# Kernel tuning notes

Hardware: AMD Instinct MI355X
Metric: run time of the kernel (lower is better)

Reference implementation:

```python
import jax, jax.numpy as jnp
import numpy as np

N_SRC = 20000
N_TGT = 20000
N_EDGE = 320000
D = 128            # in_dim == hid_dim
EDGE_IN = 2 * D + 1  # src feat + tgt feat + radial
COORD_MAX = 10.0


def _mlp2(x, w1, b1, w2, b2):
    # Linear -> SiLU -> Linear -> SiLU (edge MLP)
    h = jax.nn.silu(x @ w1 + b1)
    return jax.nn.silu(h @ w2 + b2)


def setup_inputs() -> dict:
    key = jax.random.key(0)
    ks = jax.random.split(key, 32)
    s = 0.05
    inp = {
        "src_node_feat": jax.random.normal(ks[0], (N_SRC, D), jnp.float32),
        "tgt_node_feat": jax.random.normal(ks[1], (N_TGT, D), jnp.float32),
        "src_node_coord": jax.random.normal(ks[2], (N_SRC, 3), jnp.float32),
        "tgt_node_coord": jax.random.normal(ks[3], (N_TGT, 3), jnp.float32),
        "edge_src": jax.random.randint(ks[4], (N_EDGE,), 0, N_SRC, jnp.int32),
        "edge_tgt": jax.random.randint(ks[5], (N_EDGE,), 0, N_TGT, jnp.int32),
        # edge MLP s2t
        "w1_s2t": jax.random.normal(ks[6], (EDGE_IN, D), jnp.float32) * s,
        "b1_s2t": jnp.zeros((D,), jnp.float32),
        "w2_s2t": jax.random.normal(ks[7], (D, D), jnp.float32) * s,
        "b2_s2t": jnp.zeros((D,), jnp.float32),
        # edge MLP t2s
        "w1_t2s": jax.random.normal(ks[8], (EDGE_IN, D), jnp.float32) * s,
        "b1_t2s": jnp.zeros((D,), jnp.float32),
        "w2_t2s": jax.random.normal(ks[9], (D, D), jnp.float32) * s,
        "b2_t2s": jnp.zeros((D,), jnp.float32),
        # gate MLPs (Linear(D,1) + Sigmoid)
        "wg_s2t": jax.random.normal(ks[10], (D, 1), jnp.float32) * s,
        "bg_s2t": jnp.zeros((1,), jnp.float32),
        "wg_t2s": jax.random.normal(ks[11], (D, 1), jnp.float32) * s,
        "bg_t2s": jnp.zeros((1,), jnp.float32),
        # coord MLP: Linear(D,D) + SiLU + Linear(D,1, bias=False, xavier gain 1e-3)
        "wc1": jax.random.normal(ks[12], (D, D), jnp.float32) * s,
        "bc1": jnp.zeros((D,), jnp.float32),
        "wc2": jax.random.normal(ks[13], (D, 1), jnp.float32) * 0.001,
        # node MLP tgt: Linear(2D,D) + SiLU + Linear(D,D)
        "wn1_t": jax.random.normal(ks[14], (2 * D, D), jnp.float32) * s,
        "bn1_t": jnp.zeros((D,), jnp.float32),
        "wn2_t": jax.random.normal(ks[15], (D, D), jnp.float32) * s,
        "bn2_t": jnp.zeros((D,), jnp.float32),
        # node MLP src
        "wn1_s": jax.random.normal(ks[16], (2 * D, D), jnp.float32) * s,
        "bn1_s": jnp.zeros((D,), jnp.float32),
        "wn2_s": jax.random.normal(ks[17], (D, D), jnp.float32) * s,
        "bn2_s": jnp.zeros((D,), jnp.float32),
    }
    return inp


def reference(src_node_feat, tgt_node_feat, src_node_coord, tgt_node_coord,
              edge_src, edge_tgt,
              w1_s2t, b1_s2t, w2_s2t, b2_s2t,
              w1_t2s, b1_t2s, w2_t2s, b2_t2s,
              wg_s2t, bg_s2t, wg_t2s, bg_t2s,
              wc1, bc1, wc2,
              wn1_t, bn1_t, wn2_t, bn2_t,
              wn1_s, bn1_s, wn2_s, bn2_s):
    # ---- coord2radial ----
    coord_diff = tgt_node_coord[edge_tgt] - src_node_coord[edge_src]  # [E,3]
    radial = jnp.sum(coord_diff ** 2, axis=1, keepdims=True)          # [E,1]

    # ---- edge function (gather + concat + two edge MLPs + gates) ----
    edge_in = jnp.concatenate(
        [src_node_feat[edge_src], tgt_node_feat[edge_tgt], radial], axis=1)  # [E, 257]
    e_s2t = _mlp2(edge_in, w1_s2t, b1_s2t, w2_s2t, b2_s2t)  # [E,D]
    e_t2s = _mlp2(edge_in, w1_t2s, b1_t2s, w2_t2s, b2_t2s)  # [E,D]
    e_s2t = e_s2t * jax.nn.sigmoid(e_s2t @ wg_s2t + bg_s2t)
    e_t2s = e_t2s * jax.nn.sigmoid(e_t2s @ wg_t2s + bg_t2s)

    # ---- coord update (coords_agg='mean', output_coord=True) ----
    coord_w = jax.nn.silu(e_s2t @ wc1 + bc1) @ wc2          # [E,1]
    weighted_trans = coord_diff * coord_w                   # [E,3]
    trans_sum = jax.ops.segment_sum(weighted_trans, edge_tgt, num_segments=N_TGT)
    cnt = jax.ops.segment_sum(jnp.ones((weighted_trans.shape[0],), jnp.float32),
                              edge_tgt, num_segments=N_TGT)
    agg_trans = trans_sum / jnp.maximum(cnt, 1.0)[:, None]
    tgt_coord_out = tgt_node_coord + jnp.clip(agg_trans, -COORD_MAX, COORD_MAX)

    # ---- node function (scatter-add aggregation + node MLPs + residual) ----
    agg_s2t = jax.ops.segment_sum(e_s2t, edge_tgt, num_segments=N_TGT)  # [Nt,D]
    agg_t2s = jax.ops.segment_sum(e_t2s, edge_src, num_segments=N_SRC)  # [Ns,D]
    tgt_in = jnp.concatenate([tgt_node_feat, agg_s2t], axis=1)  # [Nt,2D]
    src_in = jnp.concatenate([src_node_feat, agg_t2s], axis=1)  # [Ns,2D]
    tgt_out = jax.nn.silu(tgt_in @ wn1_t + bn1_t) @ wn2_t + bn2_t
    src_out = jax.nn.silu(src_in @ wn1_s + bn1_s) @ wn2_s + bn2_s
    tgt_out = tgt_node_feat + tgt_out  # residual (dims match)
    src_out = src_node_feat + src_out

    return src_out, tgt_out, src_node_coord, tgt_coord_out
```

## Files before the change

### kernel.cpp

```cpp
#include <hip/hip_runtime.h>

#define NN 20000
#define NEDGE 320000
#define COORD_MAX 10.0f

#define LDH 136
#define TILE_N 64
#define LDN  264

typedef __attribute__((ext_vector_type(4))) float f32x4;
typedef __attribute__((ext_vector_type(8))) short short8;
typedef __attribute__((ext_vector_type(8))) __bf16 bf16x8;

static __device__ __forceinline__ f32x4 mfma16(short8 a, short8 b, f32x4 c) {
  return __builtin_amdgcn_mfma_f32_16x16x32_bf16(
      __builtin_bit_cast(bf16x8, a), __builtin_bit_cast(bf16x8, b), c, 0, 0, 0);
}
static __device__ __forceinline__ unsigned short f2bf(float f) {
  unsigned u = __builtin_bit_cast(unsigned, f);
  u += 0x7FFFu + ((u >> 16) & 1u);
  return (unsigned short)(u >> 16);
}
static __device__ __forceinline__ float bf2f(unsigned short u) {
  unsigned x = ((unsigned)u) << 16;
  return __builtin_bit_cast(float, x);
}
static __device__ __forceinline__ unsigned cvtpk(float lo, float hi) {
  unsigned r;
  asm("v_cvt_pk_bf16_f32 %0, %1, %2" : "=v"(r) : "v"(lo), "v"(hi));
  return r;
}
static __device__ __forceinline__ float sigm(float x) {
  return __builtin_amdgcn_rcpf(1.f + __expf(-x));
}
static __device__ __forceinline__ float silu_(float x) { return x * sigm(x); }

struct PackJobs {
  const float* w[11];
  unsigned short* o[11];
  int kreal[11];
  int nk[11];
};

__global__ void egnn_pack_all(PackJobs J) {
  const int job = blockIdx.y;
  const int nk = J.nk[job];
  const int idx = blockIdx.x * 256 + threadIdx.x;
  if (idx >= nk * 512) return;
  const float* w = J.w[job];
  const int kreal = J.kreal[job];
  const int lane = idx & 63;
  const int ct = (idx >> 6) & 7;
  const int kstep = idx >> 9;
  const int col = ct * 16 + (lane & 15);
  const int k0 = kstep * 32 + (lane >> 4) * 8;
  union { short8 s; unsigned short u[8]; } t;
#pragma unroll
  for (int j = 0; j < 8; ++j) {
    int k = k0 + j;
    t.u[j] = (k < kreal) ? f2bf(w[(size_t)k * 128 + col]) : (unsigned short)0;
  }
  reinterpret_cast<short8*>(J.o[job])[idx] = t.s;
}

struct PreJobs {
  const float* x[4];
  const unsigned short* w[4];
  unsigned short* o[4];
};

__global__ __launch_bounds__(256, 2) void egnn_pre(PreJobs J, int N) {
  __shared__ __align__(16) unsigned short sX[64 * LDH];
  const int job = blockIdx.y;
  const float* X = J.x[job];
  const unsigned short* W = J.w[job];
  unsigned short* O = J.o[job];
  const int n0 = blockIdx.x * 64;
  const int tid = threadIdx.x;

  for (int s = tid; s < 64 * 32; s += 256) {
    const int row = s >> 5;
    const int c4 = (s & 31) * 4;
    const int node = n0 + row;
    float4 v = {0.f, 0.f, 0.f, 0.f};
    if (node < N) v = reinterpret_cast<const float4*>(X + (size_t)node * 128)[s & 31];
    *reinterpret_cast<uint2*>(&sX[row * LDH + c4]) =
        uint2{cvtpk(v.x, v.y), cvtpk(v.z, v.w)};
  }
  __syncthreads();

  const int lane = tid & 63, wid = tid >> 6;
  const int r16 = lane & 15, g4 = lane >> 4;
  const int rowBase = wid * 16;

  f32x4 acc[8];
#pragma unroll
  for (int ct = 0; ct < 8; ++ct) acc[ct] = f32x4{0.f, 0.f, 0.f, 0.f};
#pragma unroll
  for (int ks = 0; ks < 4; ++ks) {
    const short8 a = *reinterpret_cast<const short8*>(
        &sX[(rowBase + r16) * LDH + ks * 32 + g4 * 8]);
#pragma unroll
    for (int ct = 0; ct < 8; ++ct) {
      const short8 b = *reinterpret_cast<const short8*>(
          W + ((size_t)(ks * 8 + ct) * 64 + lane) * 8);
      acc[ct] = mfma16(a, b, acc[ct]);
    }
  }
#pragma unroll
  for (int ct = 0; ct < 8; ++ct) {
    const int col = ct * 16 + r16;
#pragma unroll
    for (int r = 0; r < 4; ++r) {
      const int node = n0 + rowBase + g4 * 4 + r;
      if (node < N) O[(size_t)node * 128 + col] = f2bf(acc[ct][r]);
    }
  }
}

__global__ void egnn_hist(const int* __restrict__ eTgt, const int* __restrict__ eSrc,
                          int* __restrict__ cntT, int* __restrict__ cntS) {
  const int e = blockIdx.x * 256 + threadIdx.x;
  if (e < NEDGE) {
    atomicAdd(&cntT[eTgt[e]], 1);
    atomicAdd(&cntS[eSrc[e]], 1);
  }
}

__global__ __launch_bounds__(1024) void egnn_scan(
    const int* __restrict__ c0, int* __restrict__ r0, int* __restrict__ o0,
    const int* __restrict__ c1, int* __restrict__ r1, int* __restrict__ o1, int n) {
  const int* cnt = blockIdx.x ? c1 : c0;
  int* rp = blockIdx.x ? r1 : r0;
  int* oc = blockIdx.x ? o1 : o0;
  __shared__ int sums[1024];
  const int tid = threadIdx.x;
  const int chunk = (n + 1023) / 1024;
  const int i0 = tid * chunk;
  int local = 0;
  for (int k = 0; k < chunk; ++k) {
    const int i = i0 + k;
    if (i < n) local += cnt[i];
  }
  sums[tid] = local;
  __syncthreads();
  for (int s = 1; s < 1024; s <<= 1) {
    int v = (tid >= s) ? sums[tid - s] : 0;
    __syncthreads();
    sums[tid] += v;
    __syncthreads();
  }
  int run = (tid == 0) ? 0 : sums[tid - 1];
  for (int k = 0; k < chunk; ++k) {
    const int i = i0 + k;
    if (i < n) { rp[i] = run; oc[i] = run; run += cnt[i]; }
  }
  if (tid == 1023) rp[n] = sums[1023];
}

__global__ void egnn_scatter(const int* __restrict__ eTgt, const int* __restrict__ eSrc,
                             int* __restrict__ offT, int* __restrict__ offS,
                             int* __restrict__ permT, int* __restrict__ permS) {
  const int e = blockIdx.x * 256 + threadIdx.x;
  if (e < NEDGE) {
    permT[atomicAdd(&offT[eTgt[e]], 1)] = e;
    permS[atomicAdd(&offS[eSrc[e]], 1)] = e;
  }
}

__global__ __launch_bounds__(256, 4) void egnn_edge(
    const unsigned short* __restrict__ S1A, const unsigned short* __restrict__ T1A,
    const unsigned short* __restrict__ S1B, const unsigned short* __restrict__ T1B,
    const float* __restrict__ srcC, const float* __restrict__ tgtC,
    const int* __restrict__ eSrc, const int* __restrict__ eTgt,
    const float* __restrict__ w1A, const float* __restrict__ b1A,
    const float* __restrict__ w1B, const float* __restrict__ b1B,
    const unsigned short* __restrict__ w2pA, const float* __restrict__ b2A,
    const float* __restrict__ wgA, const float* __restrict__ bgA,
    const unsigned short* __restrict__ w2pB, const float* __restrict__ b2B,
    const float* __restrict__ wgB, const float* __restrict__ bgB,
    const unsigned short* __restrict__ wc1p, const float* __restrict__ bc1,
    const float* __restrict__ wc2,
    const int* __restrict__ permT, const int* __restrict__ permS,
    float* __restrict__ aggA, float* __restrict__ aggB,
    float* __restrict__ wtBuf)
{
  __shared__ __align__(16) unsigned short sH[4][32 * LDH];
  __shared__ float sCD[128 * 3];
  __shared__ float sRad[128];
  __shared__ int sS[128];
  __shared__ int sT[128];

  const int dir = blockIdx.y;
  const int tid = threadIdx.x;
  const int j0 = blockIdx.x * 128;
  const int* __restrict__ perm = dir ? permS : permT;

  if (tid < 128) {
    const int e = perm[j0 + tid];
    const int s = eSrc[e], t = eTgt[e];
    sS[tid] = s; sT[tid] = t;
    const float dx = tgtC[t * 3 + 0] - srcC[s * 3 + 0];
    const float dy = tgtC[t * 3 + 1] - srcC[s * 3 + 1];
    const float dz = tgtC[t * 3 + 2] - srcC[s * 3 + 2];
    sCD[tid * 3 + 0] = dx; sCD[tid * 3 + 1] = dy; sCD[tid * 3 + 2] = dz;
    sRad[tid] = dx * dx + dy * dy + dz * dz;
  }
  __syncthreads();

  const int lane = tid & 63, wid = tid >> 6;
  const int r16 = lane & 15, g4 = lane >> 4;
  const int we = wid * 32;
  const int h32 = lane >> 5;
  const int c4 = (lane & 31) * 4;

  const unsigned short* S1 = dir ? S1B : S1A;
  const unsigned short* T1 = dir ? T1B : T1A;
  const float* w1 = dir ? w1B : w1A;
  const float* b1 = dir ? b1B : b1A;
  const float4 wr = *reinterpret_cast<const float4*>(w1 + 256 * 128 + c4);
  const float4 bb = *reinterpret_cast<const float4*>(b1 + c4);

  unsigned short* hT = sH[wid];

#pragma unroll 8
  for (int i = 0; i < 16; ++i) {
    const int row = 2 * i + h32;
    const int e = we + row;
    const int s = sS[e], t = sT[e];
    const float rad = sRad[e];
    const ushort4 a = *reinterpret_cast<const ushort4*>(S1 + (size_t)s * 128 + c4);
    const ushort4 b = *reinterpret_cast<const ushort4*>(T1 + (size_t)t * 128 + c4);
    const float f0 = silu_(bf2f(a.x) + bf2f(b.x) + rad * wr.x + bb.x);
    const float f1 = silu_(bf2f(a.y) + bf2f(b.y) + rad * wr.y + bb.y);
    const float f2 = silu_(bf2f(a.z) + bf2f(b.z) + rad * wr.z + bb.z);
    const float f3 = silu_(bf2f(a.w) + bf2f(b.w) + rad * wr.w + bb.w);
    *reinterpret_cast<uint2*>(&hT[row * LDH + c4]) =
        uint2{cvtpk(f0, f1), cvtpk(f2, f3)};
  }

  const unsigned short* w2p = dir ? w2pB : w2pA;
  f32x4 acc[2][8];
#pragma unroll
  for (int rt = 0; rt < 2; ++rt)
#pragma unroll
    for (int ct = 0; ct < 8; ++ct) acc[rt][ct] = f32x4{0.f, 0.f, 0.f, 0.f};
#pragma unroll
  for (int ks = 0; ks < 4; ++ks) {
    short8 a[2];
#pragma unroll
    for (int rt = 0; rt < 2; ++rt)
      a[rt] = *reinterpret_cast<const short8*>(
          &hT[(rt * 16 + r16) * LDH + ks * 32 + g4 * 8]);
#pragma unroll
    for (int ct = 0; ct < 8; ++ct) {
      const short8 b = *reinterpret_cast<const short8*>(
          w2p + ((size_t)(ks * 8 + ct) * 64 + lane) * 8);
#pragma unroll
      for (int rt = 0; rt < 2; ++rt) acc[rt][ct] = mfma16(a[rt], b, acc[rt][ct]);
    }
  }

  const float* b2 = dir ? b2B : b2A;
  const float* wg = dir ? wgB : wgA;
  const float bg = dir ? bgB[0] : bgA[0];
  float part[2][4];
#pragma unroll
  for (int rt = 0; rt < 2; ++rt)
#pragma unroll
    for (int r = 0; r < 4; ++r) part[rt][r] = 0.f;
#pragma unroll
  for (int ct = 0; ct < 8; ++ct) {
    const float b2v = b2[ct * 16 + r16];
    const float wgv = wg[ct * 16 + r16];
#pragma unroll
    for (int rt = 0; rt < 2; ++rt)
#pragma unroll
      for (int r = 0; r < 4; ++r) {
        const float e = silu_(acc[rt][ct][r] + b2v);
        acc[rt][ct][r] = e;
        part[rt][r] += e * wgv;
      }
  }
#pragma unroll
  for (int m = 1; m < 16; m <<= 1)
#pragma unroll
    for (int rt = 0; rt < 2; ++rt)
#pragma unroll
      for (int r = 0; r < 4; ++r) part[rt][r] += __shfl_xor(part[rt][r], m, 64);
#pragma unroll
  for (int rt = 0; rt < 2; ++rt)
#pragma unroll
    for (int r = 0; r < 4; ++r) {
      const float gate = sigm(part[rt][r] + bg);
#pragma unroll
      for (int ct = 0; ct < 8; ++ct) acc[rt][ct][r] *= gate;
    }

#pragma unroll
  for (int rt = 0; rt < 2; ++rt)
#pragma unroll
    for (int ct = 0; ct < 8; ++ct)
#pragma unroll
      for (int r = 0; r < 4; ++r)
        hT[(rt * 16 + g4 * 4 + r) * LDH + ct * 16 + r16] = f2bf(acc[rt][ct][r]);

  if (dir == 0) {
    f32x4 ac[2][8];
#pragma unroll
    for (int rt = 0; rt < 2; ++rt)
#pragma unroll
      for (int ct = 0; ct < 8; ++ct) ac[rt][ct] = f32x4{0.f, 0.f, 0.f, 0.f};
#pragma unroll
    for (int ks = 0; ks < 4; ++ks) {
      short8 a[2];
#pragma unroll
      for (int rt = 0; rt < 2; ++rt)
        a[rt] = *reinterpret_cast<const short8*>(
            &hT[(rt * 16 + r16) * LDH + ks * 32 + g4 * 8]);
#pragma unroll
      for (int ct = 0; ct < 8; ++ct) {
        const short8 b = *reinterpret_cast<const short8*>(
            wc1p + ((size_t)(ks * 8 + ct) * 64 + lane) * 8);
#pragma unroll
        for (int rt = 0; rt < 2; ++rt) ac[rt][ct] = mfma16(a[rt], b, ac[rt][ct]);
      }
    }
    float pc[2][4];
#pragma unroll
    for (int rt = 0; rt < 2; ++rt)
#pragma unroll
      for (int r = 0; r < 4; ++r) pc[rt][r] = 0.f;
#pragma unroll
    for (int ct = 0; ct < 8; ++ct) {
      const float bcv = bc1[ct * 16 + r16];
      const float w2v = wc2[ct * 16 + r16];
#pragma unroll
      for (int rt = 0; rt < 2; ++rt)
#pragma unroll
        for (int r = 0; r < 4; ++r)
          pc[rt][r] += silu_(ac[rt][ct][r] + bcv) * w2v;
    }
#pragma unroll
    for (int m = 1; m < 16; m <<= 1)
#pragma unroll
      for (int rt = 0; rt < 2; ++rt)
#pragma unroll
        for (int r = 0; r < 4; ++r) pc[rt][r] += __shfl_xor(pc[rt][r], m, 64);

#pragma unroll
    for (int rt = 0; rt < 2; ++rt)
#pragma unroll
      for (int r = 0; r < 4; ++r) {
        if (r16 == 0) {
          const int el = we + rt * 16 + g4 * 4 + r;
          const float p = pc[rt][r];
          const float4 w = {sCD[el * 3 + 0] * p, sCD[el * 3 + 1] * p,
                            sCD[el * 3 + 2] * p, 0.f};
          *reinterpret_cast<float4*>(wtBuf + (size_t)(j0 + el) * 4) = w;
        }
      }
  }

  {
    const int* __restrict__ nids = dir ? sS : sT;
    float* __restrict__ agg = dir ? aggB : aggA;
    const int c2 = lane * 2;
    float s0 = 0.f, s1 = 0.f;
    int curNode = nids[we];
    int segStart = 0;
#pragma unroll 4
    for (int row = 0; row < 32; ++row) {
      const ushort2 v = *reinterpret_cast<const ushort2*>(&hT[row * LDH + c2]);
      s0 += bf2f(v.x); s1 += bf2f(v.y);
      const int nxt = (row < 31) ? nids[we + row + 1] : -1;
      if (nxt != curNode) {
        float* dst = agg + (size_t)curNode * 128 + c2;
        if (segStart > 0 && row < 31) {
          dst[0] = s0; dst[1] = s1;
        } else {
          atomicAdd(dst, s0);
          atomicAdd(dst + 1, s1);
        }
        s0 = 0.f; s1 = 0.f;
        curNode = nxt; segStart = row + 1;
      }
    }
  }
}

__global__ void egnn_coord(const float* __restrict__ srcC, const float* __restrict__ tgtC,
                           const float* __restrict__ wt, const int* __restrict__ rp,
                           float* __restrict__ outSC, float* __restrict__ outTC) {
  const int n = blockIdx.x * 256 + threadIdx.x;
  if (n >= NN) return;
  outSC[n * 3 + 0] = srcC[n * 3 + 0];
  outSC[n * 3 + 1] = srcC[n * 3 + 1];
  outSC[n * 3 + 2] = srcC[n * 3 + 2];
  const int j0 = rp[n], j1 = rp[n + 1];
  float ax = 0.f, ay = 0.f, az = 0.f;
  for (int j = j0; j < j1; ++j) {
    const float4 v = *reinterpret_cast<const float4*>(wt + (size_t)j * 4);
    ax += v.x; ay += v.y; az += v.z;
  }
  const float c = fmaxf((float)(j1 - j0), 1.f);
  ax = fminf(fmaxf(ax / c, -COORD_MAX), COORD_MAX);
  ay = fminf(fmaxf(ay / c, -COORD_MAX), COORD_MAX);
  az = fminf(fmaxf(az / c, -COORD_MAX), COORD_MAX);
  outTC[n * 3 + 0] = tgtC[n * 3 + 0] + ax;
  outTC[n * 3 + 1] = tgtC[n * 3 + 1] + ay;
  outTC[n * 3 + 2] = tgtC[n * 3 + 2] + az;
}

struct NodeJobs {
  const float* feat[2];
  const float* agg[2];
  const unsigned short* w1p[2];
  const float* b1[2];
  const unsigned short* w2p[2];
  const float* b2[2];
  float* outp[2];
};

__global__ __launch_bounds__(256, 2) void egnn_node(NodeJobs J, int N) {
  __shared__ __align__(16) unsigned short sIn[TILE_N * LDN];
  __shared__ __align__(16) unsigned short sH2[TILE_N * LDH];
  const int job = blockIdx.y;
  const float* __restrict__ feat = J.feat[job];
  const float* __restrict__ agg = J.agg[job];
  const unsigned short* __restrict__ w1p = J.w1p[job];
  const float* __restrict__ b1 = J.b1[job];
  const unsigned short* __restrict__ w2p = J.w2p[job];
  const float* __restrict__ b2 = J.b2[job];
  float* __restrict__ outp = J.outp[job];

  const int tid = threadIdx.x;
  const int n0 = blockIdx.x * TILE_N;

  for (int s = tid; s < 64 * 64; s += 256) {
    const int row = s >> 6;
    const int half = (s >> 5) & 1;
    const int c4 = (s & 31) * 4;
    const int node = n0 + row;
    float4 v = {0.f, 0.f, 0.f, 0.f};
    if (node < N)
      v = reinterpret_cast<const float4*>((half ? agg : feat) + (size_t)node * 128)[s & 31];
    *reinterpret_cast<uint2*>(&sIn[row * LDN + half * 128 + c4]) =
        uint2{cvtpk(v.x, v.y), cvtpk(v.z, v.w)};
  }
  __syncthreads();

  const int lane = tid & 63;
  const int wid = tid >> 6;
  const int rowBase = wid * 16;
  const int r16 = lane & 15;
  const int g4 = lane >> 4;

  f32x4 acc[8];
#pragma unroll
  for (int ct = 0; ct < 8; ++ct) acc[ct] = f32x4{0.f, 0.f, 0.f, 0.f};
#pragma unroll
  for (int ks = 0; ks < 8; ++ks) {
    const short8 a = *reinterpret_cast<const short8*>(
        &sIn[(rowBase + r16) * LDN + ks * 32 + g4 * 8]);
#pragma unroll
    for (int ct = 0; ct < 8; ++ct) {
      const short8 b = *reinterpret_cast<const short8*>(
          w1p + ((size_t)(ks * 8 + ct) * 64 + lane) * 8);
      acc[ct] = mfma16(a, b, acc[ct]);
    }
  }
#pragma unroll
  for (int ct = 0; ct < 8; ++ct) {
    const int col = ct * 16 + r16;
    const float bias = b1[col];
#pragma unroll
    for (int r = 0; r < 4; ++r) {
      const float h = silu_(acc[ct][r] + bias);
      sH2[(rowBase + g4 * 4 + r) * LDH + col] = f2bf(h);
    }
  }

  f32x4 acc2[8];
#pragma unroll
  for (int ct = 0; ct < 8; ++ct) acc2[ct] = f32x4{0.f, 0.f, 0.f, 0.f};
#pragma unroll
  for (int ks = 0; ks < 4; ++ks) {
    const short8 a = *reinterpret_cast<const short8*>(
        &sH2[(rowBase + r16) * LDH + ks * 32 + g4 * 8]);
#pragma unroll
    for (int ct = 0; ct < 8; ++ct) {
      const short8 b = *reinterpret_cast<const short8*>(
          w2p + ((size_t)(ks * 8 + ct) * 64 + lane) * 8);
      acc2[ct] = mfma16(a, b, acc2[ct]);
    }
  }

#pragma unroll
  for (int ct = 0; ct < 8; ++ct) {
    const int col = ct * 16 + r16;
    const float bias = b2[col];
#pragma unroll
    for (int r = 0; r < 4; ++r) {
      const int node = n0 + rowBase + g4 * 4 + r;
      if (node < N)
        outp[(size_t)node * 128 + col] = feat[(size_t)node * 128 + col] + acc2[ct][r] + bias;
    }
  }
}

extern "C" void kernel_launch(void* const* d_in, const int* in_sizes, int n_in,
                              void* d_out, int out_size, void* d_ws, size_t ws_size,
                              hipStream_t stream) {
  const float* srcF = (const float*)d_in[0];
  const float* tgtF = (const float*)d_in[1];
  const float* srcC = (const float*)d_in[2];
  const float* tgtC = (const float*)d_in[3];
  const int* eSrc = (const int*)d_in[4];
  const int* eTgt = (const int*)d_in[5];
  const float* w1_s2t = (const float*)d_in[6];
  const float* b1_s2t = (const float*)d_in[7];
  const float* w2_s2t = (const float*)d_in[8];
  const float* b2_s2t = (const float*)d_in[9];
  const float* w1_t2s = (const float*)d_in[10];
  const float* b1_t2s = (const float*)d_in[11];
  const float* w2_t2s = (const float*)d_in[12];
  const float* b2_t2s = (const float*)d_in[13];
  const float* wg_s2t = (const float*)d_in[14];
  const float* bg_s2t = (const float*)d_in[15];
  const float* wg_t2s = (const float*)d_in[16];
  const float* bg_t2s = (const float*)d_in[17];
  const float* wc1 = (const float*)d_in[18];
  const float* bc1 = (const float*)d_in[19];
  const float* wc2 = (const float*)d_in[20];
  const float* wn1_t = (const float*)d_in[21];
  const float* bn1_t = (const float*)d_in[22];
  const float* wn2_t = (const float*)d_in[23];
  const float* bn2_t = (const float*)d_in[24];
  const float* wn1_s = (const float*)d_in[25];
  const float* bn1_s = (const float*)d_in[26];
  const float* wn2_s = (const float*)d_in[27];
  const float* bn2_s = (const float*)d_in[28];

  char* ws = (char*)d_ws;
  size_t off = 0;
  auto take = [&](size_t bytes) -> char* {
    char* p = ws + off;
    off = (off + bytes + 255) & ~(size_t)255;
    return p;
  };
  float* aggA = (float*)take((size_t)NN * 128 * 4);
  float* aggB = (float*)take((size_t)NN * 128 * 4);
  float* wtBuf = (float*)take((size_t)NEDGE * 4 * 4);
  unsigned short* S1A = (unsigned short*)take((size_t)NN * 128 * 2);
  unsigned short* T1A = (unsigned short*)take((size_t)NN * 128 * 2);
  unsigned short* S1B = (unsigned short*)take((size_t)NN * 128 * 2);
  unsigned short* T1B = (unsigned short*)take((size_t)NN * 128 * 2);
  unsigned short* w1tA = (unsigned short*)take(4 * 4096 * 2);
  unsigned short* w1mA = (unsigned short*)take(4 * 4096 * 2);
  unsigned short* w1tB = (unsigned short*)take(4 * 4096 * 2);
  unsigned short* w1mB = (unsigned short*)take(4 * 4096 * 2);
  unsigned short* w2pA = (unsigned short*)take(4 * 4096 * 2);
  unsigned short* w2pB = (unsigned short*)take(4 * 4096 * 2);
  unsigned short* wc1p = (unsigned short*)take(4 * 4096 * 2);
  unsigned short* wn1pt = (unsigned short*)take(8 * 4096 * 2);
  unsigned short* wn2pt = (unsigned short*)take(4 * 4096 * 2);
  unsigned short* wn1ps = (unsigned short*)take(8 * 4096 * 2);
  unsigned short* wn2ps = (unsigned short*)take(4 * 4096 * 2);
  int* cntT = (int*)take((size_t)NN * 4);
  int* cntS = (int*)take((size_t)NN * 4);
  const char* cntZeroStart = (const char*)cntT;
  const size_t cntZeroBytes = (size_t)((char*)cntS + NN * 4 - (char*)cntT);
  int* rowptrT = (int*)take((size_t)(NN + 1) * 4);
  int* rowptrS = (int*)take((size_t)(NN + 1) * 4);
  int* offT = (int*)take((size_t)NN * 4);
  int* offS = (int*)take((size_t)NN * 4);
  int* permT = (int*)take((size_t)NEDGE * 4);
  int* permS = (int*)take((size_t)NEDGE * 4);

  hipMemsetAsync(aggA, 0, (size_t)NN * 128 * 4 * 2, stream);
  hipMemsetAsync((void*)cntZeroStart, 0, cntZeroBytes, stream);

  PackJobs PJ;
  PJ.w[0] = w1_s2t;             PJ.o[0] = w1tA;  PJ.kreal[0] = 128; PJ.nk[0] = 4;
  PJ.w[1] = w1_s2t + 128 * 128; PJ.o[1] = w1mA;  PJ.kreal[1] = 128; PJ.nk[1] = 4;
  PJ.w[2] = w1_t2s;             PJ.o[2] = w1tB;  PJ.kreal[2] = 128; PJ.nk[2] = 4;
  PJ.w[3] = w1_t2s + 128 * 128; PJ.o[3] = w1mB;  PJ.kreal[3] = 128; PJ.nk[3] = 4;
  PJ.w[4] = w2_s2t;             PJ.o[4] = w2pA;  PJ.kreal[4] = 128; PJ.nk[4] = 4;
  PJ.w[5] = w2_t2s;             PJ.o[5] = w2pB;  PJ.kreal[5] = 128; PJ.nk[5] = 4;
  PJ.w[6] = wc1;                PJ.o[6] = wc1p;  PJ.kreal[6] = 128; PJ.nk[6] = 4;
  PJ.w[7] = wn1_t;              PJ.o[7] = wn1pt; PJ.kreal[7] = 256; PJ.nk[7] = 8;
  PJ.w[8] = wn2_t;              PJ.o[8] = wn2pt; PJ.kreal[8] = 128; PJ.nk[8] = 4;
  PJ.w[9] = wn1_s;              PJ.o[9] = wn1ps; PJ.kreal[9] = 256; PJ.nk[9] = 8;
  PJ.w[10] = wn2_s;             PJ.o[10] = wn2ps; PJ.kreal[10] = 128; PJ.nk[10] = 4;
  egnn_pack_all<<<dim3(16, 11), 256, 0, stream>>>(PJ);

  PreJobs PR;
  PR.x[0] = srcF; PR.w[0] = w1tA; PR.o[0] = S1A;
  PR.x[1] = tgtF; PR.w[1] = w1mA; PR.o[1] = T1A;
  PR.x[2] = srcF; PR.w[2] = w1tB; PR.o[2] = S1B;
  PR.x[3] = tgtF; PR.w[3] = w1mB; PR.o[3] = T1B;
  egnn_pre<<<dim3(313, 4), 256, 0, stream>>>(PR, NN);

  egnn_hist<<<NEDGE / 256, 256, 0, stream>>>(eTgt, eSrc, cntT, cntS);
  egnn_scan<<<2, 1024, 0, stream>>>(cntT, rowptrT, offT, cntS, rowptrS, offS, NN);
  egnn_scatter<<<NEDGE / 256, 256, 0, stream>>>(eTgt, eSrc, offT, offS, permT, permS);

  float* outSrc = (float*)d_out;
  float* outTgt = outSrc + (size_t)NN * 128;
  float* outSC  = outTgt + (size_t)NN * 128;
  float* outTC  = outSC + (size_t)NN * 3;

  egnn_edge<<<dim3(NEDGE / 128, 2), 256, 0, stream>>>(
      S1A, T1A, S1B, T1B, srcC, tgtC, eSrc, eTgt,
      w1_s2t, b1_s2t, w1_t2s, b1_t2s,
      w2pA, b2_s2t, wg_s2t, bg_s2t,
      w2pB, b2_t2s, wg_t2s, bg_t2s,
      wc1p, bc1, wc2, permT, permS, aggA, aggB, wtBuf);

  egnn_coord<<<(NN + 255) / 256, 256, 0, stream>>>(
      srcC, tgtC, wtBuf, rowptrT, outSC, outTC);

  NodeJobs NJ;
  NJ.feat[0] = tgtF; NJ.agg[0] = aggA;
  NJ.w1p[0] = wn1pt; NJ.b1[0] = bn1_t; NJ.w2p[0] = wn2pt; NJ.b2[0] = bn2_t;
  NJ.outp[0] = outTgt;
  NJ.feat[1] = srcF; NJ.agg[1] = aggB;
  NJ.w1p[1] = wn1ps; NJ.b1[1] = bn1_s; NJ.w2p[1] = wn2ps; NJ.b2[1] = bn2_s;
  NJ.outp[1] = outSrc;

  const int nodeBlocks = (NN + TILE_N - 1) / TILE_N;
  egnn_node<<<dim3(nodeBlocks, 2), 256, 0, stream>>>(NJ, NN);
}
```

Measured before the change: 320.9 us.

## Merge small kernels, fold first-layer bias into precompute, widen edge gather loads

Histogram, weight packing and aggregation zeroing now run in one prep launch. The coordinate reduction moves into the node kernel as a third grid row, which removes launches and the separate memset. The pre-projection now processes both directions per block, reusing the staged input tile, and adds the first-layer bias into the target projection so the edge kernel no longer adds it. The edge gather uses 16-byte loads of 8 bf16 values per lane instead of 8-byte loads. The prep grid is much larger, and most blocks in the pack rows exit immediately, which adds some idle work.

```diff
diff --git a/kernel.cpp b/kernel.cpp
--- a/kernel.cpp
+++ b/kernel.cpp
@@ -42,39 +42,56 @@
   int nk[11];
 };
 
-__global__ void egnn_pack_all(PackJobs J) {
+__global__ void egnn_prep(PackJobs J,
+                          const int* __restrict__ eTgt, const int* __restrict__ eSrc,
+                          int* __restrict__ cntT, int* __restrict__ cntS,
+                          float* __restrict__ aggZero ) {
   const int job = blockIdx.y;
-  const int nk = J.nk[job];
   const int idx = blockIdx.x * 256 + threadIdx.x;
-  if (idx >= nk * 512) return;
-  const float* w = J.w[job];
-  const int kreal = J.kreal[job];
-  const int lane = idx & 63;
-  const int ct = (idx >> 6) & 7;
-  const int kstep = idx >> 9;
-  const int col = ct * 16 + (lane & 15);
-  const int k0 = kstep * 32 + (lane >> 4) * 8;
-  union { short8 s; unsigned short u[8]; } t;
-#pragma unroll
-  for (int j = 0; j < 8; ++j) {
-    int k = k0 + j;
-    t.u[j] = (k < kreal) ? f2bf(w[(size_t)k * 128 + col]) : (unsigned short)0;
-  }
-  reinterpret_cast<short8*>(J.o[job])[idx] = t.s;
+  if (job < 11) {
+    const int nk = J.nk[job];
+    if (idx >= nk * 512) return;
+    const float* w = J.w[job];
+    const int kreal = J.kreal[job];
+    const int lane = idx & 63;
+    const int ct = (idx >> 6) & 7;
+    const int kstep = idx >> 9;
+    const int col = ct * 16 + (lane & 15);
+    const int k0 = kstep * 32 + (lane >> 4) * 8;
+    union { short8 s; unsigned short u[8]; } t;
+#pragma unroll
+    for (int j = 0; j < 8; ++j) {
+      int k = k0 + j;
+      t.u[j] = (k < kreal) ? f2bf(w[(size_t)k * 128 + col]) : (unsigned short)0;
+    }
+    reinterpret_cast<short8*>(J.o[job])[idx] = t.s;
+  } else if (job == 11) {
+    if (idx < NEDGE) {
+      atomicAdd(&cntT[eTgt[idx]], 1);
+      atomicAdd(&cntS[eSrc[idx]], 1);
+    }
+  } else {
+    float4* p = reinterpret_cast<float4*>(aggZero);
+    const int total = 2 * NN * 128 / 4;
+    for (int k = idx; k < total; k += 1250 * 256)
+      p[k] = float4{0.f, 0.f, 0.f, 0.f};
+  }
 }
 
 struct PreJobs {
-  const float* x[4];
-  const unsigned short* w[4];
-  unsigned short* o[4];
+  const float* x[2];
+  const unsigned short* wA[2];
+  const unsigned short* wB[2];
+  const float* biasA[2];
+  const float* biasB[2];
+  unsigned short* oA[2];
+  unsigned short* oB[2];
 };
 
 __global__ __launch_bounds__(256, 2) void egnn_pre(PreJobs J, int N) {
   __shared__ __align__(16) unsigned short sX[64 * LDH];
   const int job = blockIdx.y;
-  const float* X = J.x[job];
-  const unsigned short* W = J.w[job];
-  unsigned short* O = J.o[job];
+  const float* __restrict__ X = J.x[job];
   const int n0 = blockIdx.x * 64;
   const int tid = threadIdx.x;
 
@@ -93,37 +110,35 @@
   const int r16 = lane & 15, g4 = lane >> 4;
   const int rowBase = wid * 16;
 
-  f32x4 acc[8];
-#pragma unroll
-  for (int ct = 0; ct < 8; ++ct) acc[ct] = f32x4{0.f, 0.f, 0.f, 0.f};
-#pragma unroll
-  for (int ks = 0; ks < 4; ++ks) {
-    const short8 a = *reinterpret_cast<const short8*>(
-        &sX[(rowBase + r16) * LDH + ks * 32 + g4 * 8]);
+#pragma unroll 1
+  for (int half = 0; half < 2; ++half) {
+    const unsigned short* __restrict__ W = half ? J.wB[job] : J.wA[job];
+    const float* __restrict__ bias = half ? J.biasB[job] : J.biasA[job];
+    unsigned short* __restrict__ O = half ? J.oB[job] : J.oA[job];
+    f32x4 acc[8];
+#pragma unroll
+    for (int ct = 0; ct < 8; ++ct) acc[ct] = f32x4{0.f, 0.f, 0.f, 0.f};
+#pragma unroll
+    for (int ks = 0; ks < 4; ++ks) {
+      const short8 a = *reinterpret_cast<const short8*>(
+          &sX[(rowBase + r16) * LDH + ks * 32 + g4 * 8]);
+#pragma unroll
+      for (int ct = 0; ct < 8; ++ct) {
+        const short8 b = *reinterpret_cast<const short8*>(
+            W + ((size_t)(ks * 8 + ct) * 64 + lane) * 8);
+        acc[ct] = mfma16(a, b, acc[ct]);
+      }
+    }
 #pragma unroll
     for (int ct = 0; ct < 8; ++ct) {
-      const short8 b = *reinterpret_cast<const short8*>(
-          W + ((size_t)(ks * 8 + ct) * 64 + lane) * 8);
-      acc[ct] = mfma16(a, b, acc[ct]);
-    }
-  }
-#pragma unroll
-  for (int ct = 0; ct < 8; ++ct) {
-    const int col = ct * 16 + r16;
-#pragma unroll
-    for (int r = 0; r < 4; ++r) {
-      const int node = n0 + rowBase + g4 * 4 + r;
-      if (node < N) O[(size_t)node * 128 + col] = f2bf(acc[ct][r]);
-    }
-  }
-}
-
-__global__ void egnn_hist(const int* __restrict__ eTgt, const int* __restrict__ eSrc,
-                          int* __restrict__ cntT, int* __restrict__ cntS) {
-  const int e = blockIdx.x * 256 + threadIdx.x;
-  if (e < NEDGE) {
-    atomicAdd(&cntT[eTgt[e]], 1);
-    atomicAdd(&cntS[eSrc[e]], 1);
+      const int col = ct * 16 + r16;
+      const float bv = bias ? bias[col] : 0.f;
+#pragma unroll
+      for (int r = 0; r < 4; ++r) {
+        const int node = n0 + rowBase + g4 * 4 + r;
+        if (node < N) O[(size_t)node * 128 + col] = f2bf(acc[ct][r] + bv);
+      }
+    }
   }
 }
 
@@ -173,8 +188,7 @@
     const unsigned short* __restrict__ S1B, const unsigned short* __restrict__ T1B,
     const float* __restrict__ srcC, const float* __restrict__ tgtC,
     const int* __restrict__ eSrc, const int* __restrict__ eTgt,
-    const float* __restrict__ w1A, const float* __restrict__ b1A,
-    const float* __restrict__ w1B, const float* __restrict__ b1B,
+    const float* __restrict__ w1A, const float* __restrict__ w1B,
     const unsigned short* __restrict__ w2pA, const float* __restrict__ b2A,
     const float* __restrict__ wgA, const float* __restrict__ bgA,
     const unsigned short* __restrict__ w2pB, const float* __restrict__ b2B,
@@ -213,30 +227,42 @@
   const int we = wid * 32;
   const int h32 = lane >> 5;
   const int c4 = (lane & 31) * 4;
-
-  const unsigned short* S1 = dir ? S1B : S1A;
-  const unsigned short* T1 = dir ? T1B : T1A;
+  const int c8 = (lane & 15) * 8;
+  const int r4 = lane >> 4;
+  const int c2 = lane * 2;
+
+  const unsigned short* __restrict__ S1 = dir ? S1B : S1A;
+  const unsigned short* __restrict__ T1 = dir ? T1B : T1A;
   const float* w1 = dir ? w1B : w1A;
-  const float* b1 = dir ? b1B : b1A;
-  const float4 wr = *reinterpret_cast<const float4*>(w1 + 256 * 128 + c4);
-  const float4 bb = *reinterpret_cast<const float4*>(b1 + c4);
+  const float4 wr0 = *reinterpret_cast<const float4*>(w1 + 256 * 128 + c8);
+  const float4 wr1 = *reinterpret_cast<const float4*>(w1 + 256 * 128 + c8 + 4);
+  const float* b2 = dir ? b2B : b2A;
+  const float* wg = dir ? wgB : wgA;
+  const float bg = dir ? bgB[0] : bgA[0];
+  const int* __restrict__ nids = dir ? sS : sT;
+  float* __restrict__ agg = dir ? aggB : aggA;
 
   unsigned short* hT = sH[wid];
 
-#pragma unroll 8
-  for (int i = 0; i < 16; ++i) {
-    const int row = 2 * i + h32;
+#pragma unroll
+  for (int i = 0; i < 8; ++i) {
+    const int row = 4 * i + r4;
     const int e = we + row;
     const int s = sS[e], t = sT[e];
     const float rad = sRad[e];
-    const ushort4 a = *reinterpret_cast<const ushort4*>(S1 + (size_t)s * 128 + c4);
-    const ushort4 b = *reinterpret_cast<const ushort4*>(T1 + (size_t)t * 128 + c4);
-    const float f0 = silu_(bf2f(a.x) + bf2f(b.x) + rad * wr.x + bb.x);
-    const float f1 = silu_(bf2f(a.y) + bf2f(b.y) + rad * wr.y + bb.y);
-    const float f2 = silu_(bf2f(a.z) + bf2f(b.z) + rad * wr.z + bb.z);
-    const float f3 = silu_(bf2f(a.w) + bf2f(b.w) + rad * wr.w + bb.w);
-    *reinterpret_cast<uint2*>(&hT[row * LDH + c4]) =
-        uint2{cvtpk(f0, f1), cvtpk(f2, f3)};
+    union { short8 v; unsigned short u[8]; } a, b;
+    a.v = *reinterpret_cast<const short8*>(S1 + (size_t)s * 128 + c8);
+    b.v = *reinterpret_cast<const short8*>(T1 + (size_t)t * 128 + c8);
+    const float f0 = silu_(bf2f(a.u[0]) + bf2f(b.u[0]) + rad * wr0.x);
+    const float f1 = silu_(bf2f(a.u[1]) + bf2f(b.u[1]) + rad * wr0.y);
+    const float f2 = silu_(bf2f(a.u[2]) + bf2f(b.u[2]) + rad * wr0.z);
+    const float f3 = silu_(bf2f(a.u[3]) + bf2f(b.u[3]) + rad * wr0.w);
+    const float f4 = silu_(bf2f(a.u[4]) + bf2f(b.u[4]) + rad * wr1.x);
+    const float f5 = silu_(bf2f(a.u[5]) + bf2f(b.u[5]) + rad * wr1.y);
+    const float f6 = silu_(bf2f(a.u[6]) + bf2f(b.u[6]) + rad * wr1.z);
+    const float f7 = silu_(bf2f(a.u[7]) + bf2f(b.u[7]) + rad * wr1.w);
+    *reinterpret_cast<uint4*>(&hT[row * LDH + c8]) =
+        uint4{cvtpk(f0, f1), cvtpk(f2, f3), cvtpk(f4, f5), cvtpk(f6, f7)};
   }
 
   const unsigned short* w2p = dir ? w2pB : w2pA;
@@ -261,9 +287,6 @@
     }
   }
 
-  const float* b2 = dir ? b2B : b2A;
-  const float* wg = dir ? wgB : wgA;
-  const float bg = dir ? bgB[0] : bgA[0];
   float part[2][4];
 #pragma unroll
   for (int rt = 0; rt < 2; ++rt)
@@ -363,9 +386,6 @@
   }
 
   {
-    const int* __restrict__ nids = dir ? sS : sT;
-    float* __restrict__ agg = dir ? aggB : aggA;
-    const int c2 = lane * 2;
     float s0 = 0.f, s1 = 0.f;
     int curNode = nids[we];
     int segStart = 0;
@@ -389,29 +409,6 @@
   }
 }
 
-__global__ void egnn_coord(const float* __restrict__ srcC, const float* __restrict__ tgtC,
-                           const float* __restrict__ wt, const int* __restrict__ rp,
-                           float* __restrict__ outSC, float* __restrict__ outTC) {
-  const int n = blockIdx.x * 256 + threadIdx.x;
-  if (n >= NN) return;
-  outSC[n * 3 + 0] = srcC[n * 3 + 0];
-  outSC[n * 3 + 1] = srcC[n * 3 + 1];
-  outSC[n * 3 + 2] = srcC[n * 3 + 2];
-  const int j0 = rp[n], j1 = rp[n + 1];
-  float ax = 0.f, ay = 0.f, az = 0.f;
-  for (int j = j0; j < j1; ++j) {
-    const float4 v = *reinterpret_cast<const float4*>(wt + (size_t)j * 4);
-    ax += v.x; ay += v.y; az += v.z;
-  }
-  const float c = fmaxf((float)(j1 - j0), 1.f);
-  ax = fminf(fmaxf(ax / c, -COORD_MAX), COORD_MAX);
-  ay = fminf(fmaxf(ay / c, -COORD_MAX), COORD_MAX);
-  az = fminf(fmaxf(az / c, -COORD_MAX), COORD_MAX);
-  outTC[n * 3 + 0] = tgtC[n * 3 + 0] + ax;
-  outTC[n * 3 + 1] = tgtC[n * 3 + 1] + ay;
-  outTC[n * 3 + 2] = tgtC[n * 3 + 2] + az;
-}
-
 struct NodeJobs {
   const float* feat[2];
   const float* agg[2];
@@ -422,10 +419,39 @@
   float* outp[2];
 };
 
-__global__ __launch_bounds__(256, 2) void egnn_node(NodeJobs J, int N) {
+__global__ __launch_bounds__(256, 2) void egnn_node(
+    NodeJobs J, int N,
+    const float* __restrict__ srcC, const float* __restrict__ tgtC,
+    const float* __restrict__ wt, const int* __restrict__ rp,
+    float* __restrict__ outSC, float* __restrict__ outTC) {
   __shared__ __align__(16) unsigned short sIn[TILE_N * LDN];
   __shared__ __align__(16) unsigned short sH2[TILE_N * LDH];
   const int job = blockIdx.y;
+  const int tid = threadIdx.x;
+
+  if (job == 2) {
+    const int n = blockIdx.x * 256 + tid;
+    if (n < NN) {
+      outSC[n * 3 + 0] = srcC[n * 3 + 0];
+      outSC[n * 3 + 1] = srcC[n * 3 + 1];
+      outSC[n * 3 + 2] = srcC[n * 3 + 2];
+      const int j0 = rp[n], j1 = rp[n + 1];
+      float ax = 0.f, ay = 0.f, az = 0.f;
+      for (int j = j0; j < j1; ++j) {
+        const float4 v = *reinterpret_cast<const float4*>(wt + (size_t)j * 4);
+        ax += v.x; ay += v.y; az += v.z;
+      }
+      const float c = fmaxf((float)(j1 - j0), 1.f);
+      ax = fminf(fmaxf(ax / c, -COORD_MAX), COORD_MAX);
+      ay = fminf(fmaxf(ay / c, -COORD_MAX), COORD_MAX);
+      az = fminf(fmaxf(az / c, -COORD_MAX), COORD_MAX);
+      outTC[n * 3 + 0] = tgtC[n * 3 + 0] + ax;
+      outTC[n * 3 + 1] = tgtC[n * 3 + 1] + ay;
+      outTC[n * 3 + 2] = tgtC[n * 3 + 2] + az;
+    }
+    return;
+  }
+
   const float* __restrict__ feat = J.feat[job];
   const float* __restrict__ agg = J.agg[job];
   const unsigned short* __restrict__ w1p = J.w1p[job];
@@ -434,7 +460,6 @@
   const float* __restrict__ b2 = J.b2[job];
   float* __restrict__ outp = J.outp[job];
 
-  const int tid = threadIdx.x;
   const int n0 = blockIdx.x * TILE_N;
 
   for (int s = tid; s < 64 * 64; s += 256) {
@@ -578,7 +603,6 @@
   int* permT = (int*)take((size_t)NEDGE * 4);
   int* permS = (int*)take((size_t)NEDGE * 4);
 
-  hipMemsetAsync(aggA, 0, (size_t)NN * 128 * 4 * 2, stream);
   hipMemsetAsync((void*)cntZeroStart, 0, cntZeroBytes, stream);
 
   PackJobs PJ;
@@ -593,16 +617,17 @@
   PJ.w[8] = wn2_t;              PJ.o[8] = wn2pt; PJ.kreal[8] = 128; PJ.nk[8] = 4;
   PJ.w[9] = wn1_s;              PJ.o[9] = wn1ps; PJ.kreal[9] = 256; PJ.nk[9] = 8;
   PJ.w[10] = wn2_s;             PJ.o[10] = wn2ps; PJ.kreal[10] = 128; PJ.nk[10] = 4;
-  egnn_pack_all<<<dim3(16, 11), 256, 0, stream>>>(PJ);
+  egnn_prep<<<dim3(1250, 13), 256, 0, stream>>>(PJ, eTgt, eSrc, cntT, cntS, aggA);
 
   PreJobs PR;
-  PR.x[0] = srcF; PR.w[0] = w1tA; PR.o[0] = S1A;
-  PR.x[1] = tgtF; PR.w[1] = w1mA; PR.o[1] = T1A;
-  PR.x[2] = srcF; PR.w[2] = w1tB; PR.o[2] = S1B;
-  PR.x[3] = tgtF; PR.w[3] = w1mB; PR.o[3] = T1B;
-  egnn_pre<<<dim3(313, 4), 256, 0, stream>>>(PR, NN);
-
-  egnn_hist<<<NEDGE / 256, 256, 0, stream>>>(eTgt, eSrc, cntT, cntS);
+  PR.x[0] = srcF; PR.wA[0] = w1tA; PR.wB[0] = w1tB;
+  PR.biasA[0] = nullptr; PR.biasB[0] = nullptr;
+  PR.oA[0] = S1A; PR.oB[0] = S1B;
+  PR.x[1] = tgtF; PR.wA[1] = w1mA; PR.wB[1] = w1mB;
+  PR.biasA[1] = b1_s2t; PR.biasB[1] = b1_t2s;
+  PR.oA[1] = T1A; PR.oB[1] = T1B;
+  egnn_pre<<<dim3(313, 2), 256, 0, stream>>>(PR, NN);
+
   egnn_scan<<<2, 1024, 0, stream>>>(cntT, rowptrT, offT, cntS, rowptrS, offS, NN);
   egnn_scatter<<<NEDGE / 256, 256, 0, stream>>>(eTgt, eSrc, offT, offS, permT, permS);
 
@@ -613,13 +638,10 @@
 
   egnn_edge<<<dim3(NEDGE / 128, 2), 256, 0, stream>>>(
       S1A, T1A, S1B, T1B, srcC, tgtC, eSrc, eTgt,
-      w1_s2t, b1_s2t, w1_t2s, b1_t2s,
+      w1_s2t, w1_t2s,
       w2pA, b2_s2t, wg_s2t, bg_s2t,
       w2pB, b2_t2s, wg_t2s, bg_t2s,
       wc1p, bc1, wc2, permT, permS, aggA, aggB, wtBuf);
-
-  egnn_coord<<<(NN + 255) / 256, 256, 0, stream>>>(
-      srcC, tgtC, wtBuf, rowptrT, outSC, outTC);
 
   NodeJobs NJ;
   NJ.feat[0] = tgtF; NJ.agg[0] = aggA;
@@ -630,5 +652,6 @@
   NJ.outp[1] = outSrc;
 
   const int nodeBlocks = (NN + TILE_N - 1) / TILE_N;
-  egnn_node<<<dim3(nodeBlocks, 2), 256, 0, stream>>>(NJ, NN);
-}
+  egnn_node<<<dim3(nodeBlocks, 3), 256, 0, stream>>>(
+      NJ, NN, srcC, tgtC, wtBuf, rowptrT, outSC, outTC);
+}
```

After: 306.3 us. 4.6% less time.
